# Kernel optimization log

Measured on AMD Instinct MI355X. Metric: run time of the kernel, lower is better.

The kernel has to match this reference:

```python
import jax, jax.numpy as jnp
import numpy as np
from jax import lax

D = 512      # inter_dim
E = 768      # expand_dim
S = 256      # squeeze_dim
BUCKET = 64
N_BLOCK = 6

def layernorm(x, g, b, eps):
    m = jnp.mean(x, axis=-1, keepdims=True)
    v = jnp.mean(jnp.square(x - m), axis=-1, keepdims=True)
    return (x - m) / jnp.sqrt(v + eps) * g + b

def setup_inputs():
    key = jax.random.key(0)
    ks = jax.random.split(key, 12)
    B, N, IN = 4, 4096, 768
    def rn(k, shape, scale):
        return jax.random.normal(k, shape, dtype=jnp.float32) * scale
    return {
        "xs": jax.random.normal(ks[0], (B, N, IN), dtype=jnp.float32),
        # in1: Linear(IN, D) + LayerNorm(eps=1e-8) + LeakyReLU(0.1)
        "W_in": rn(ks[1], (IN, D), IN ** -0.5), "b_in": jnp.zeros(D),
        "ln_in_g": jnp.ones(D), "ln_in_b": jnp.zeros(D),
        # 6 GAU (FlashQuadAttention) blocks, params stacked on leading axis
        "blk_ln_g": jnp.ones((N_BLOCK, D)), "blk_ln_b": jnp.zeros((N_BLOCK, D)),
        "blk_Wuv": rn(ks[2], (N_BLOCK, D, 2 * E + S), D ** -0.5),
        "blk_buv": jnp.zeros((N_BLOCK, 2 * E + S)),
        "blk_gamma": jnp.ones((N_BLOCK, 2, S)) + rn(ks[3], (N_BLOCK, 2, S), 0.02),
        "blk_beta": rn(ks[4], (N_BLOCK, 2, S), 0.02),
        "blk_Wo": rn(ks[5], (N_BLOCK, E, D), E ** -0.5),
        "blk_bo": jnp.zeros((N_BLOCK, D)),
        # tr_layer (applied inside tree loop)
        "tr_W": rn(ks[6], (D, D), D ** -0.5), "tr_b": jnp.zeros(D),
        "tr_a": jnp.full((), 1e-6, dtype=jnp.float32),
        # out1 = TransLayer + Linear(D, out_dim)
        "tr2_W": rn(ks[7], (D, D), D ** -0.5), "tr2_b": jnp.zeros(D),
        "tr2_a": jnp.full((), 1e-6, dtype=jnp.float32),
        "out_W": rn(ks[8], (D, 2), D ** -0.5), "out_b": jnp.zeros(2),
    }

def reference(xs, W_in, b_in, ln_in_g, ln_in_b,
              blk_ln_g, blk_ln_b, blk_Wuv, blk_buv, blk_gamma, blk_beta,
              blk_Wo, blk_bo, tr_W, tr_b, tr_a, tr2_W, tr2_b, tr2_a,
              out_W, out_b):
    def subnet(h):  # h: [n_buckets, BUCKET, D]
        def step(h, p):
            lg, lb, Wuv, buv, gam, bet, Wo, bo = p
            n = layernorm(h, lg, lb, 1e-5)
            uvb = jax.nn.silu(n @ Wuv + buv)
            u, v, base = uvb[..., :E], uvb[..., E:2 * E], uvb[..., 2 * E:]
            q = base * gam[0] + bet[0]
            k = base * gam[1] + bet[1]
            Lq = h.shape[1]
            a = jnp.square(jax.nn.relu(jnp.einsum('gls,gms->glm', q, k) / Lq))
            o = jnp.einsum('glm,gme->gle', a, v) * u
            return h + o @ Wo + bo, None
        h, _ = lax.scan(step, h, (blk_ln_g, blk_ln_b, blk_Wuv, blk_buv,
                                  blk_gamma, blk_beta, blk_Wo, blk_bo))
        return h

    def tr_layer(x, W, b, a):
        return x + jax.nn.gelu(x @ W + b, approximate=False) * a

    def run_sample(x):  # x: [N, in_dim]
        h = layernorm(x @ W_in + b_in, ln_in_g, ln_in_b, 1e-8)
        h = jnp.where(h > 0, h, 0.1 * h)  # LeakyReLU(0.1)
        seq = h
        ys = []
        while seq.shape[0] > 1:  # static shapes -> unrolled tree levels
            ids = jnp.argsort(jnp.linalg.norm(seq, axis=-1))  # sort by L2 norm
            buckets = seq[ids].reshape(-1, BUCKET, D)
            gy = subnet(buckets).mean(axis=1)           # [n_buckets, D]
            ys.append(tr_layer(gy, tr_W, tr_b, tr_a).mean(axis=0))
            seq = gy
        return jnp.stack(ys, 0).mean(0)  # [D]

    y = jax.vmap(run_sample)(xs)          # [B, D]
    y = tr_layer(y, tr2_W, tr2_b, tr2_a)  # out1 TransLayer
    return y @ out_W + out_b              # [B, out_dim]
```

## Files before the change

kernel.cpp:

```cpp
#include <hip/hip_runtime.h>
#include <math.h>

#define R1C 16384

enum { OP_STORE = 0, OP_SILU = 1, OP_RESID = 2, OP_TR = 3 };

typedef _Float16 f16x8 __attribute__((ext_vector_type(8)));
typedef float f32x4 __attribute__((ext_vector_type(4)));

__device__ __forceinline__ float silu_f(float x) { return x / (1.0f + __expf(-x)); }
__device__ __forceinline__ float gelu_f(float x) {
  return 0.5f * x * (1.0f + erff(x * 0.70710678118654752f));
}

__device__ __forceinline__ void gll16(const void* g, const void* l) {
  __builtin_amdgcn_global_load_lds(
      (const __attribute__((address_space(1))) unsigned int*)g,
      (__attribute__((address_space(3))) unsigned int*)l, 16, 0, 0);
}

__device__ __forceinline__ void xcd_swizzle(int& bx, int& by) {
  int nx = gridDim.x;
  int nwg = nx * gridDim.y;
  int flat = by * nx + bx;
  int q = nwg >> 3, r = nwg & 7;
  int xcd = flat & 7, pos = flat >> 3;
  int lbid = (xcd < r) ? xcd * (q + 1) + pos
                       : r * (q + 1) + (xcd - r) * q + pos;
  bx = lbid % nx;
  by = lbid / nx;
}


__global__ __launch_bounds__(512) void gemm_f16(
    const _Float16* __restrict__ A, int lda,
    const _Float16* __restrict__ Bt, int ldb,
    float* __restrict__ C, int ldc, int K,
    const float* __restrict__ bias, int mode,
    const int* __restrict__ ids)
{
  const int BUF = 128 * 32;
  __shared__ _Float16 As[3 * BUF];
  __shared__ _Float16 Bs[3 * BUF];
  int bx = blockIdx.x, by = blockIdx.y;
  xcd_swizzle(bx, by);
  int tid = threadIdx.x;
  int lane = tid & 63, w = tid >> 6;
  int wm = w >> 1, wn = w & 1;
  int row0 = by * 128, col0 = bx * 128;

  int m0 = tid >> 2;
  int k0e = (((tid & 3) - (m0 >> 1)) & 3) * 8;
  const _Float16* gA0 = A + (size_t)(row0 + m0) * lda + k0e;
  const _Float16* gB0 = Bt + (size_t)(col0 + m0) * ldb + k0e;
  const _Float16* lA0 = As + (size_t)(w * 64) * 8;
  const _Float16* lB0 = Bs + (size_t)(w * 64) * 8;

  int mrow = lane & 15, quad = lane >> 4;
  const f16x8* aptr[2];
  const f16x8* bptr[4];
#pragma unroll
  for (int t = 0; t < 2; ++t) {
    int ml = wm * 32 + t * 16 + mrow;
    aptr[t] = (const f16x8*)(As + (size_t)(ml * 4 + ((quad + (ml >> 1)) & 3)) * 8);
  }
#pragma unroll
  for (int nt = 0; nt < 4; ++nt) {
    int nl = wn * 64 + nt * 16 + mrow;
    bptr[nt] = (const f16x8*)(Bs + (size_t)(nl * 4 + ((quad + (nl >> 1)) & 3)) * 8);
  }

  f32x4 acc[2][4] = {};

  int ntile = K >> 5;
  gll16(gA0, lA0); gll16(gB0, lB0);
  gA0 += 32; gB0 += 32;
  if (ntile > 1) {
    gll16(gA0, lA0 + BUF); gll16(gB0, lB0 + BUF);
    gA0 += 32; gB0 += 32;
  }

  int cur = 0;
  for (int t = 0; t < ntile; ++t) {
    if (t + 1 < ntile) asm volatile("s_waitcnt vmcnt(2)" ::: "memory");
    else               asm volatile("s_waitcnt vmcnt(0)" ::: "memory");
    __builtin_amdgcn_s_barrier();
    __builtin_amdgcn_sched_barrier(0);
    if (t + 2 < ntile) {
      int pf = cur + 2; if (pf >= 3) pf -= 3;
      gll16(gA0, lA0 + pf * BUF); gll16(gB0, lB0 + pf * BUF);
      gA0 += 32; gB0 += 32;
    }
    int fo = cur * (BUF / 8);
    f16x8 af[2], bfr[4];
#pragma unroll
    for (int tt = 0; tt < 2; ++tt) af[tt] = *(aptr[tt] + fo);
#pragma unroll
    for (int nt = 0; nt < 4; ++nt) bfr[nt] = *(bptr[nt] + fo);
#pragma unroll
    for (int mt = 0; mt < 2; ++mt)
#pragma unroll
      for (int nt = 0; nt < 4; ++nt)
        acc[mt][nt] = __builtin_amdgcn_mfma_f32_16x16x32_f16(
            af[mt], bfr[nt], acc[mt][nt], 0, 0, 0);
    cur = (cur == 2) ? 0 : cur + 1;
  }

#pragma unroll
  for (int mt = 0; mt < 2; ++mt) {
#pragma unroll
    for (int nt = 0; nt < 4; ++nt) {
      int c = col0 + wn * 64 + nt * 16 + mrow;
      float bv = bias ? bias[c] : 0.0f;
#pragma unroll
      for (int reg = 0; reg < 4; ++reg) {
        int r = row0 + wm * 32 + mt * 16 + quad * 4 + reg;
        float val = acc[mt][nt][reg] + bv;
        if (mode == OP_STORE) {
          C[(size_t)r * ldc + c] = val;
        } else if (mode == OP_SILU) {
          C[(size_t)r * ldc + c] = silu_f(val);
        } else {
          int hr = ids ? ids[r] : r;
          C[(size_t)hr * ldc + c] += val;
        }
      }
    }
  }
}

__global__ __launch_bounds__(512) void gemm_f16_split(
    const _Float16* __restrict__ Ah, const _Float16* __restrict__ Al, int lda,
    const _Float16* __restrict__ Bh, const _Float16* __restrict__ Bl, int ldb,
    float* __restrict__ C, int ldc, int K, const float* __restrict__ bias)
{
  const int BUF = 128 * 32;
  __shared__ _Float16 AsH[2 * BUF], AsL[2 * BUF];
  __shared__ _Float16 BsH[2 * BUF], BsL[2 * BUF];
  int bx = blockIdx.x, by = blockIdx.y;
  xcd_swizzle(bx, by);
  int tid = threadIdx.x;
  int lane = tid & 63, w = tid >> 6;
  int wm = w >> 1, wn = w & 1;
  int row0 = by * 128, col0 = bx * 128;

  int m0 = tid >> 2;
  int k0e = (((tid & 3) - (m0 >> 1)) & 3) * 8;
  size_t a0 = (size_t)(row0 + m0) * lda + k0e;
  size_t b0 = (size_t)(col0 + m0) * ldb + k0e;
  size_t l0 = (size_t)(w * 64) * 8;

  int mrow = lane & 15, quad = lane >> 4;
  size_t aoff[2], boff[4];
#pragma unroll
  for (int t = 0; t < 2; ++t) {
    int ml = wm * 32 + t * 16 + mrow;
    aoff[t] = (size_t)(ml * 4 + ((quad + (ml >> 1)) & 3)) * 8;
  }
#pragma unroll
  for (int nt = 0; nt < 4; ++nt) {
    int nl = wn * 64 + nt * 16 + mrow;
    boff[nt] = (size_t)(nl * 4 + ((quad + (nl >> 1)) & 3)) * 8;
  }

  f32x4 acc[2][4] = {};

  gll16(Ah + a0, AsH + l0); gll16(Al + a0, AsL + l0);
  gll16(Bh + b0, BsH + l0); gll16(Bl + b0, BsL + l0);
  a0 += 32; b0 += 32;

  for (int kt = 0; kt < K; kt += 32) {
    int cur = (kt >> 5) & 1;
    __syncthreads();
    if (kt + 32 < K) {
      size_t o = (size_t)(cur ^ 1) * BUF;
      gll16(Ah + a0, AsH + l0 + o); gll16(Al + a0, AsL + l0 + o);
      gll16(Bh + b0, BsH + l0 + o); gll16(Bl + b0, BsL + l0 + o);
      a0 += 32; b0 += 32;
    }
    size_t o = (size_t)cur * BUF;
    f16x8 ah[2], al_[2], bh[4], bl[4];
#pragma unroll
    for (int t = 0; t < 2; ++t) {
      ah[t]  = *(const f16x8*)(AsH + aoff[t] + o);
      al_[t] = *(const f16x8*)(AsL + aoff[t] + o);
    }
#pragma unroll
    for (int nt = 0; nt < 4; ++nt) {
      bh[nt] = *(const f16x8*)(BsH + boff[nt] + o);
      bl[nt] = *(const f16x8*)(BsL + boff[nt] + o);
    }
#pragma unroll
    for (int mt = 0; mt < 2; ++mt)
#pragma unroll
      for (int nt = 0; nt < 4; ++nt) {
        acc[mt][nt] = __builtin_amdgcn_mfma_f32_16x16x32_f16(
            ah[mt], bh[nt], acc[mt][nt], 0, 0, 0);
        acc[mt][nt] = __builtin_amdgcn_mfma_f32_16x16x32_f16(
            ah[mt], bl[nt], acc[mt][nt], 0, 0, 0);
        acc[mt][nt] = __builtin_amdgcn_mfma_f32_16x16x32_f16(
            al_[mt], bh[nt], acc[mt][nt], 0, 0, 0);
      }
  }

#pragma unroll
  for (int mt = 0; mt < 2; ++mt)
#pragma unroll
    for (int nt = 0; nt < 4; ++nt) {
      int c = col0 + wn * 64 + nt * 16 + mrow;
      float bv = bias ? bias[c] : 0.0f;
#pragma unroll
      for (int reg = 0; reg < 4; ++reg) {
        int r = row0 + wm * 32 + mt * 16 + quad * 4 + reg;
        C[(size_t)r * ldc + c] = acc[mt][nt][reg] + bv;
      }
    }
}

__global__ __launch_bounds__(512) void gemm_f16_uvb(
    const _Float16* __restrict__ A, int lda,
    const _Float16* __restrict__ Bt,
    int c0, int nu,
    _Float16* __restrict__ ub, _Float16* __restrict__ vb, float* __restrict__ baseb,
    int CH, int K, const float* __restrict__ buv)
{
  const int BUF = 128 * 32;
  __shared__ _Float16 As[3 * BUF];
  __shared__ _Float16 Bs[3 * BUF];
  int bx = blockIdx.x, by = blockIdx.y;
  xcd_swizzle(bx, by);
  int tid = threadIdx.x;
  int lane = tid & 63, w = tid >> 6;
  int wm = w >> 1, wn = w & 1;
  int row0 = by * 128;

  int x = bx;
  int xl, regbase, ldc_, is_base = 0;
  _Float16* dst16 = nullptr;
  if (x < nu)            { xl = x;          regbase = c0;        dst16 = ub; ldc_ = CH; }
  else if (x < 2 * nu)   { xl = x - nu;     regbase = 768 + c0;  dst16 = vb; ldc_ = CH; }
  else                   { xl = x - 2 * nu; regbase = 1536;      is_base = 1; ldc_ = 256; }
  int brow0 = regbase + xl * 128;
  int dcol0 = xl * 128;

  int m0 = tid >> 2;
  int k0e = (((tid & 3) - (m0 >> 1)) & 3) * 8;
  const _Float16* gA0 = A + (size_t)(row0 + m0) * lda + k0e;
  const _Float16* gB0 = Bt + (size_t)(brow0 + m0) * 512 + k0e;
  const _Float16* lA0 = As + (size_t)(w * 64) * 8;
  const _Float16* lB0 = Bs + (size_t)(w * 64) * 8;

  int mrow = lane & 15, quad = lane >> 4;
  const f16x8* aptr[2];
  const f16x8* bptr[4];
#pragma unroll
  for (int t = 0; t < 2; ++t) {
    int ml = wm * 32 + t * 16 + mrow;
    aptr[t] = (const f16x8*)(As + (size_t)(ml * 4 + ((quad + (ml >> 1)) & 3)) * 8);
  }
#pragma unroll
  for (int nt = 0; nt < 4; ++nt) {
    int nl = wn * 64 + nt * 16 + mrow;
    bptr[nt] = (const f16x8*)(Bs + (size_t)(nl * 4 + ((quad + (nl >> 1)) & 3)) * 8);
  }

  f32x4 acc[2][4] = {};

  int ntile = K >> 5;
  gll16(gA0, lA0); gll16(gB0, lB0);
  gA0 += 32; gB0 += 32;
  if (ntile > 1) {
    gll16(gA0, lA0 + BUF); gll16(gB0, lB0 + BUF);
    gA0 += 32; gB0 += 32;
  }

  int cur = 0;
  for (int t = 0; t < ntile; ++t) {
    if (t + 1 < ntile) asm volatile("s_waitcnt vmcnt(2)" ::: "memory");
    else               asm volatile("s_waitcnt vmcnt(0)" ::: "memory");
    __builtin_amdgcn_s_barrier();
    __builtin_amdgcn_sched_barrier(0);
    if (t + 2 < ntile) {
      int pf = cur + 2; if (pf >= 3) pf -= 3;
      gll16(gA0, lA0 + pf * BUF); gll16(gB0, lB0 + pf * BUF);
      gA0 += 32; gB0 += 32;
    }
    int fo = cur * (BUF / 8);
    f16x8 af[2], bfr[4];
#pragma unroll
    for (int tt = 0; tt < 2; ++tt) af[tt] = *(aptr[tt] + fo);
#pragma unroll
    for (int nt = 0; nt < 4; ++nt) bfr[nt] = *(bptr[nt] + fo);
#pragma unroll
    for (int mt = 0; mt < 2; ++mt)
#pragma unroll
      for (int nt = 0; nt < 4; ++nt)
        acc[mt][nt] = __builtin_amdgcn_mfma_f32_16x16x32_f16(
            af[mt], bfr[nt], acc[mt][nt], 0, 0, 0);
    cur = (cur == 2) ? 0 : cur + 1;
  }

#pragma unroll
  for (int mt = 0; mt < 2; ++mt) {
#pragma unroll
    for (int nt = 0; nt < 4; ++nt) {
      int lc = wn * 64 + nt * 16 + mrow;
      float bv = buv[brow0 + lc];
#pragma unroll
      for (int reg = 0; reg < 4; ++reg) {
        int r = row0 + wm * 32 + mt * 16 + quad * 4 + reg;
        float val = silu_f(acc[mt][nt][reg] + bv);
        if (is_base) baseb[(size_t)r * 256 + dcol0 + lc] = val;
        else         dst16[(size_t)r * ldc_ + dcol0 + lc] = (_Float16)val;
      }
    }
  }
}

__global__ __launch_bounds__(256) void attnapply_fused(
    const float* __restrict__ base, const float* __restrict__ gb,
    const float* __restrict__ bb, const _Float16* __restrict__ v,
    const _Float16* __restrict__ u, _Float16* __restrict__ t, int CH, int ech)
{
  __shared__ _Float16 smem[3 * 64 * 72];
  _Float16* qs = smem;
  _Float16* ks = smem + 64 * 72;
  _Float16* al = smem + 2 * 64 * 72;
  _Float16* vT = smem;

  int bx = blockIdx.x, by = blockIdx.y;
  xcd_swizzle(bx, by);
  int g = by, tid = threadIdx.x;
  int e_lo = bx * ech, e_hi = e_lo + ech;
  int lane = tid & 63, w = tid >> 6;
  int mrow = lane & 15, quad = lane >> 4;
  int srow = tid >> 2, scol = (tid & 3) * 16;

  f32x4 acc[4] = {};
  for (int s0 = 0; s0 < 256; s0 += 64) {
    const float* bp = base + ((size_t)g * 64 + srow) * 256 + s0 + scol;
#pragma unroll
    for (int j4 = 0; j4 < 4; ++j4) {
      float4 xv = *(const float4*)(bp + j4 * 4);
      float xx[4] = {xv.x, xv.y, xv.z, xv.w};
#pragma unroll
      for (int j = 0; j < 4; ++j) {
        int s = s0 + scol + j4 * 4 + j;
        qs[srow * 72 + scol + j4 * 4 + j] = (_Float16)(xx[j] * gb[s] + bb[s]);
        ks[srow * 72 + scol + j4 * 4 + j] = (_Float16)(xx[j] * gb[256 + s] + bb[256 + s]);
      }
    }
    __syncthreads();
#pragma unroll
    for (int ks2 = 0; ks2 < 2; ++ks2) {
      f16x8 aq = *(const f16x8*)(qs + (w * 16 + mrow) * 72 + ks2 * 32 + quad * 8);
#pragma unroll
      for (int nt = 0; nt < 4; ++nt) {
        f16x8 bk = *(const f16x8*)(ks + (nt * 16 + mrow) * 72 + ks2 * 32 + quad * 8);
        acc[nt] = __builtin_amdgcn_mfma_f32_16x16x32_f16(aq, bk, acc[nt], 0, 0, 0);
      }
    }
    __syncthreads();
  }
#pragma unroll
  for (int nt = 0; nt < 4; ++nt)
#pragma unroll
    for (int reg = 0; reg < 4; ++reg) {
      float val = acc[nt][reg] * (1.0f / 64.0f);
      val = val > 0.0f ? val : 0.0f;
      val = val * val;
      al[(w * 16 + quad * 4 + reg) * 72 + nt * 16 + mrow] = (_Float16)val;
    }
  __syncthreads();

  for (int e0 = e_lo; e0 < e_hi; e0 += 64) {
    const _Float16* vp = v + ((size_t)g * 64 + srow) * CH + e0 + scol;
    f16x8 x0 = *(const f16x8*)vp;
    f16x8 x1 = *(const f16x8*)(vp + 8);
#pragma unroll
    for (int j = 0; j < 8; ++j) {
      vT[(scol + j) * 72 + srow] = x0[j];
      vT[(scol + 8 + j) * 72 + srow] = x1[j];
    }
    __syncthreads();
    f32x4 acc2[4] = {};
#pragma unroll
    for (int ks2 = 0; ks2 < 2; ++ks2) {
      f16x8 af = *(const f16x8*)(al + (w * 16 + mrow) * 72 + ks2 * 32 + quad * 8);
#pragma unroll
      for (int nt = 0; nt < 4; ++nt) {
        f16x8 bf = *(const f16x8*)(vT + (nt * 16 + mrow) * 72 + ks2 * 32 + quad * 8);
        acc2[nt] = __builtin_amdgcn_mfma_f32_16x16x32_f16(af, bf, acc2[nt], 0, 0, 0);
      }
    }
#pragma unroll
    for (int nt = 0; nt < 4; ++nt)
#pragma unroll
      for (int reg = 0; reg < 4; ++reg) {
        int row = w * 16 + quad * 4 + reg;
        int col = e0 + nt * 16 + mrow;
        size_t idx = ((size_t)g * 64 + row) * CH + col;
        t[idx] = (_Float16)(acc2[nt][reg] * (float)u[idx]);
      }
    __syncthreads();
  }
}

__global__ __launch_bounds__(256) void gemm_f32(
    const float* __restrict__ A, int lda,
    const float* __restrict__ B, int ldb,
    float* __restrict__ C, int ldc,
    int M, int N, int K,
    const float* __restrict__ bias, int mode,
    const int* __restrict__ ids,
    const float* __restrict__ X,
    const float* __restrict__ alpha)
{
  __shared__ float As[16][68];
  __shared__ float Bs[16][68];
  int tid = threadIdx.x;
  int tx = tid & 15, ty = tid >> 4;
  int col0 = blockIdx.x * 64, row0 = blockIdx.y * 64;
  float acc[4][4] = {};
  int arow = tid >> 2;
  int ak   = (tid & 3) * 4;
  int bk   = tid >> 4;
  int bn   = (tid & 15) * 4;

  for (int kt = 0; kt < K; kt += 16) {
    float4 av = make_float4(0.f, 0.f, 0.f, 0.f);
    if (row0 + arow < M)
      av = *(const float4*)&A[(size_t)(row0 + arow) * lda + kt + ak];
    As[ak + 0][arow] = av.x; As[ak + 1][arow] = av.y;
    As[ak + 2][arow] = av.z; As[ak + 3][arow] = av.w;
    float4 bv = *(const float4*)&B[(size_t)(kt + bk) * ldb + col0 + bn];
    *(float4*)&Bs[bk][bn] = bv;
    __syncthreads();
#pragma unroll
    for (int k = 0; k < 16; ++k) {
      const float4 a4 = *(const float4*)&As[k][ty * 4];
      const float4 b4 = *(const float4*)&Bs[k][tx * 4];
      float a_[4] = {a4.x, a4.y, a4.z, a4.w};
      float b_[4] = {b4.x, b4.y, b4.z, b4.w};
#pragma unroll
      for (int i = 0; i < 4; ++i)
#pragma unroll
        for (int j = 0; j < 4; ++j)
          acc[i][j] = fmaf(a_[i], b_[j], acc[i][j]);
    }
    __syncthreads();
  }

#pragma unroll
  for (int i = 0; i < 4; ++i) {
    int r = row0 + ty * 4 + i;
    if (r >= M) continue;
#pragma unroll
    for (int j = 0; j < 4; ++j) {
      int c = col0 + tx * 4 + j;
      float val = acc[i][j] + (bias ? bias[c] : 0.0f);
      if (mode == OP_STORE) {
        C[(size_t)r * ldc + c] = val;
      } else if (mode == OP_SILU) {
        C[(size_t)r * ldc + c] = silu_f(val);
      } else if (mode == OP_RESID) {
        int hr = ids ? ids[r] : r;
        C[(size_t)hr * ldc + c] += val;
      } else {
        C[(size_t)r * ldc + c] = X[(size_t)r * ldc + c] + gelu_f(val) * alpha[0];
      }
    }
  }
}

__global__ __launch_bounds__(256) void transpose_cast(
    const float* __restrict__ in, _Float16* __restrict__ out, int K, int N)
{
  in  += (size_t)blockIdx.z * K * N;
  out += (size_t)blockIdx.z * K * N;
  __shared__ float t[32][33];
  int k0 = blockIdx.y * 32, n0 = blockIdx.x * 32;
  int tx = threadIdx.x & 31, ty = threadIdx.x >> 5;
  for (int i = ty; i < 32; i += 8) {
    int k = k0 + i, n = n0 + tx;
    t[i][tx] = (k < K && n < N) ? in[(size_t)k * N + n] : 0.0f;
  }
  __syncthreads();
  for (int i = ty; i < 32; i += 8) {
    int n = n0 + i, k = k0 + tx;
    if (n < N && k < K) out[(size_t)n * K + k] = (_Float16)t[tx][i];
  }
}

__global__ __launch_bounds__(256) void transpose_split(
    const float* __restrict__ in, _Float16* __restrict__ hi,
    _Float16* __restrict__ lo, int K, int N)
{
  __shared__ float t[32][33];
  int k0 = blockIdx.y * 32, n0 = blockIdx.x * 32;
  int tx = threadIdx.x & 31, ty = threadIdx.x >> 5;
  for (int i = ty; i < 32; i += 8) {
    int k = k0 + i, n = n0 + tx;
    t[i][tx] = (k < K && n < N) ? in[(size_t)k * N + n] : 0.0f;
  }
  __syncthreads();
  for (int i = ty; i < 32; i += 8) {
    int n = n0 + i, k = k0 + tx;
    if (n < N && k < K) {
      float x = t[tx][i];
      _Float16 h = (_Float16)x;
      hi[(size_t)n * K + k] = h;
      lo[(size_t)n * K + k] = (_Float16)(x - (float)h);
    }
  }
}

__global__ __launch_bounds__(256) void split_f16_kernel(
    const float* __restrict__ in, _Float16* __restrict__ hi,
    _Float16* __restrict__ lo, int n)
{
  int i = blockIdx.x * 256 + threadIdx.x;
  if (i < n) {
    float x = in[i];
    _Float16 h = (_Float16)x;
    hi[i] = h;
    lo[i] = (_Float16)(x - (float)h);
  }
}

template <typename OUT>
__global__ __launch_bounds__(256) void ln_kernel(
    const float* __restrict__ src, const int* __restrict__ ids,
    OUT* __restrict__ dst, const float* __restrict__ g,
    const float* __restrict__ b, float eps, int leaky,
    float* __restrict__ nrm2)
{
  int r = blockIdx.x;
  int sr = ids ? ids[r] : r;
  int tid = threadIdx.x;
  float v0 = src[(size_t)sr * 512 + tid];
  float v1 = src[(size_t)sr * 512 + tid + 256];
  __shared__ float red[256], red2[256];
  red[tid] = v0 + v1;
  red2[tid] = v0 * v0 + v1 * v1;
  __syncthreads();
  for (int s = 128; s > 0; s >>= 1) {
    if (tid < s) { red[tid] += red[tid + s]; red2[tid] += red2[tid + s]; }
    __syncthreads();
  }
  float mean = red[0] * (1.0f / 512.0f);
  float var  = red2[0] * (1.0f / 512.0f) - mean * mean;
  float rs = rsqrtf(var + eps);
  float o0 = (v0 - mean) * rs * g[tid] + b[tid];
  float o1 = (v1 - mean) * rs * g[tid + 256] + b[tid + 256];
  if (leaky) {
    o0 = o0 > 0.0f ? o0 : 0.1f * o0;
    o1 = o1 > 0.0f ? o1 : 0.1f * o1;
  }
  dst[(size_t)r * 512 + tid] = (OUT)o0;
  dst[(size_t)r * 512 + tid + 256] = (OUT)o1;
  if (nrm2) {
    __syncthreads();
    red[tid] = o0 * o0 + o1 * o1;
    __syncthreads();
    for (int s = 128; s > 0; s >>= 1) {
      if (tid < s) red[tid] += red[tid + s];
      __syncthreads();
    }
    if (tid == 0) nrm2[r] = red[0];
  }
}

__global__ __launch_bounds__(128) void permute_rows(
    const float* __restrict__ src, const int* __restrict__ ids,
    float* __restrict__ dst)
{
  int r = blockIdx.x, sr = ids[r];
  const float4* s = (const float4*)(src + (size_t)sr * 512);
  float4* d = (float4*)(dst + (size_t)r * 512);
  d[threadIdx.x] = s[threadIdx.x];
}

__global__ __launch_bounds__(1024) void sort_kernel(const float* __restrict__ norm2,
                                                    int* __restrict__ ids)
{
  __shared__ float key[4096];
  __shared__ int   val[4096];
  int s = blockIdx.x, tid = threadIdx.x;
  for (int i = tid; i < 4096; i += 1024) { key[i] = norm2[s * 4096 + i]; val[i] = i; }
  __syncthreads();
  for (int len = 2; len <= 4096; len <<= 1) {
    for (int j = len >> 1; j > 0; j >>= 1) {
      for (int t = tid; t < 2048; t += 1024) {
        int i1 = (t << 1) - (t & (j - 1));
        int i2 = i1 + j;
        bool up = ((i1 & len) == 0);
        float ka = key[i1], kb = key[i2];
        int va = val[i1], vb = val[i2];
        bool gt = (ka > kb) || (ka == kb && va > vb);
        if (gt == up) {
          key[i1] = kb; key[i2] = ka;
          val[i1] = vb; val[i2] = va;
        }
      }
      __syncthreads();
    }
  }
  for (int i = tid; i < 4096; i += 1024) ids[s * 4096 + i] = s * 4096 + val[i];
}

__global__ __launch_bounds__(256) void bucketmean_kernel(
    const float* __restrict__ src, const int* __restrict__ ids,
    float* __restrict__ dst)
{
  int g = blockIdx.x, tid = threadIdx.x;
  float s0 = 0.0f, s1 = 0.0f;
  for (int i = 0; i < 64; ++i) {
    int r = g * 64 + i;
    if (ids) r = ids[r];
    s0 += src[(size_t)r * 512 + tid];
    s1 += src[(size_t)r * 512 + tid + 256];
  }
  dst[(size_t)g * 512 + tid] = s0 * (1.0f / 64.0f);
  dst[(size_t)g * 512 + tid + 256] = s1 * (1.0f / 64.0f);
}

__global__ void avg_kernel(const float* __restrict__ a, const float* __restrict__ b,
                           float* __restrict__ o, int n)
{
  int i = blockIdx.x * 256 + threadIdx.x;
  if (i < n) o[i] = 0.5f * (a[i] + b[i]);
}

__global__ void out_kernel(const float* __restrict__ y, const float* __restrict__ W,
                           const float* __restrict__ b, float* __restrict__ out)
{
  int tid = threadIdx.x;
  if (tid < 8) {
    int s = tid >> 1, j = tid & 1;
    float acc = b[j];
    for (int d = 0; d < 512; ++d) acc += y[s * 512 + d] * W[d * 2 + j];
    out[s * 2 + j] = acc;
  }
}

extern "C" void kernel_launch(void* const* d_in, const int* in_sizes, int n_in,
                              void* d_out, int out_size, void* d_ws, size_t ws_size,
                              hipStream_t stream)
{
  const float* xs       = (const float*)d_in[0];
  const float* W_in     = (const float*)d_in[1];
  const float* b_in     = (const float*)d_in[2];
  const float* ln_in_g  = (const float*)d_in[3];
  const float* ln_in_b  = (const float*)d_in[4];
  const float* blk_ln_g = (const float*)d_in[5];
  const float* blk_ln_b = (const float*)d_in[6];
  const float* blk_Wuv  = (const float*)d_in[7];
  const float* blk_buv  = (const float*)d_in[8];
  const float* blk_gam  = (const float*)d_in[9];
  const float* blk_bet  = (const float*)d_in[10];
  const float* blk_Wo   = (const float*)d_in[11];
  const float* blk_bo   = (const float*)d_in[12];
  const float* tr_W     = (const float*)d_in[13];
  const float* tr_b     = (const float*)d_in[14];
  const float* tr_a     = (const float*)d_in[15];
  const float* tr2_W    = (const float*)d_in[16];
  const float* tr2_b    = (const float*)d_in[17];
  const float* tr2_a    = (const float*)d_in[18];
  const float* out_W    = (const float*)d_in[19];
  const float* out_b    = (const float*)d_in[20];
  float* outp = (float*)d_out;

  const size_t R1 = R1C;

  char* wsb = (char*)d_ws;
  size_t off = 0;
  auto carve = [&](size_t bytes) {
    char* r = wsb + off;
    off = (off + bytes + 255) & ~(size_t)255;
    return (void*)r;
  };
  float* h      = (float*)carve(R1 * 512 * 4);
  float* hslot  = (float*)carve(R1 * 512 * 4);
  float* norm2b = (float*)carve(R1 * 4);
  int*   idsb   = (int*)carve(R1 * 4);
  float* gy     = (float*)carve((size_t)256 * 512 * 4);
  float* tl     = (float*)carve((size_t)256 * 512 * 4);
  float* gy2    = (float*)carve(4 * 512 * 4);
  float* ys0    = (float*)carve(4 * 512 * 4);
  float* ys1    = (float*)carve(4 * 512 * 4);
  float* yv     = (float*)carve(4 * 512 * 4);
  float* y2     = (float*)carve(4 * 512 * 4);
  _Float16* Wuvt = (_Float16*)carve((size_t)6 * 1792 * 512 * 2);
  _Float16* Wot  = (_Float16*)carve((size_t)6 * 512 * 768 * 2);
  size_t persistent = off;

  size_t stageA_sorted = 2 * R1 * 768 * 2 + 2 * (size_t)512 * 768 * 2 + R1 * 512 * 4 + 2048;
  size_t block768 = R1 * 256 * 4 + 3 * R1 * (size_t)768 * 2 + 2048;
  size_t un_sorted = stageA_sorted > block768 ? stageA_sorted : block768;
  bool sorted_mode = (persistent + un_sorted + 4096 <= ws_size);

  int CH = 768;
  bool splitA = true;
  if (!sorted_mode) {
    size_t stageA_fb = 2 * R1 * 768 * 2 + 2 * (size_t)512 * 768 * 2 + 1024;
    auto block_bytes = [&](size_t ch) {
      return R1 * 256 * 4 + 3 * R1 * ch * 2 + 2048;
    };
    CH = 0; splitA = false;
    const int cand[4] = {768, 384, 256, 128};
    for (int ci = 0; ci < 4; ++ci) {
      size_t bb2 = block_bytes(cand[ci]);
      size_t un2 = bb2 > stageA_fb ? bb2 : stageA_fb;
      if (persistent + un2 + 4096 <= ws_size) { CH = cand[ci]; splitA = true; break; }
    }
    if (!CH) {
      for (int ci = 0; ci < 4; ++ci)
        if (persistent + block_bytes(cand[ci]) + 4096 <= ws_size) { CH = cand[ci]; break; }
      if (!CH) CH = 128;
    }
  }
  int nu = CH / 128;
  int ech = CH >= 256 ? 256 : CH;
  int nch = CH / ech;

  char* un = wsb + ((persistent + 255) & ~(size_t)255);
  _Float16* xs_hi = (_Float16*)un;
  _Float16* xs_lo = xs_hi + R1 * 768;
  _Float16* Wt_hi = xs_lo + R1 * 768;
  _Float16* Wt_lo = Wt_hi + (size_t)512 * 768;
  float*    nbA   = sorted_mode ? (float*)(Wt_lo + (size_t)512 * 768) : hslot;
  float*    baseb = (float*)un;
  _Float16* ub    = (_Float16*)(un + R1 * 256 * 4);
  _Float16* vb    = ub + R1 * (size_t)CH;
  _Float16* tb    = vb + R1 * (size_t)CH;
  _Float16* nbuf  = sorted_mode ? tb : (_Float16*)hslot;
  float* hres = sorted_mode ? hslot : h;
  const int* blkids = sorted_mode ? nullptr : idsb;

  dim3 blk(256);
  dim3 blk5(512);

  transpose_cast<<<dim3(56, 16, 6), blk, 0, stream>>>(blk_Wuv, Wuvt, 512, 1792);
  transpose_cast<<<dim3(16, 24, 6), blk, 0, stream>>>(blk_Wo, Wot, 768, 512);

  if (splitA) {
    split_f16_kernel<<<(int)(R1 * 768 / 256), blk, 0, stream>>>(xs, xs_hi, xs_lo,
                                                                (int)(R1 * 768));
    transpose_split<<<dim3(16, 24, 1), blk, 0, stream>>>(W_in, Wt_hi, Wt_lo, 768, 512);
    gemm_f16_split<<<dim3(4, 128), blk5, 0, stream>>>(xs_hi, xs_lo, 768,
        Wt_hi, Wt_lo, 768, nbA, 512, 768, b_in);
  } else {
    gemm_f32<<<dim3(8, 256), blk, 0, stream>>>(xs, 768, W_in, 512, nbA, 512,
        16384, 512, 768, b_in, OP_STORE, nullptr, nullptr, nullptr);
  }
  ln_kernel<float><<<16384, 256, 0, stream>>>(nbA, nullptr, h, ln_in_g, ln_in_b,
                                              1e-8f, 1, norm2b);
  sort_kernel<<<4, 1024, 0, stream>>>(norm2b, idsb);
  if (sorted_mode)
    permute_rows<<<16384, 128, 0, stream>>>(h, idsb, hres);

  for (int b = 0; b < 6; ++b) {
    const _Float16* Wuv_t = Wuvt + (size_t)b * 1792 * 512;
    const float*    buv   = blk_buv + b * 1792;
    const _Float16* Wo_t  = Wot + (size_t)b * 512 * 768;
    ln_kernel<_Float16><<<16384, 256, 0, stream>>>(hres, blkids, nbuf,
        blk_ln_g + b * 512, blk_ln_b + b * 512, 1e-5f, 0, nullptr);
    for (int c0 = 0; c0 < 768; c0 += CH) {
      int incl = (c0 == 0) ? 2 : 0;
      gemm_f16_uvb<<<dim3(2 * nu + incl, 128), blk5, 0, stream>>>(nbuf, 512, Wuv_t,
          c0, nu, ub, vb, baseb, CH, 512, buv);
      attnapply_fused<<<dim3(nch, 256), blk, 0, stream>>>(baseb, blk_gam + b * 512,
          blk_bet + b * 512, vb, ub, tb, CH, ech);
      const float* bo = (c0 + CH == 768) ? (blk_bo + b * 512) : nullptr;
      gemm_f16<<<dim3(4, 128), blk5, 0, stream>>>(tb, CH, Wo_t + c0, 768,
          hres, 512, CH, bo, OP_RESID, blkids);
    }
  }
  bucketmean_kernel<<<256, 256, 0, stream>>>(hres, blkids, gy);

  gemm_f32<<<dim3(8, 4), blk, 0, stream>>>(gy, 512, tr_W, 512, tl, 512,
      256, 512, 512, tr_b, OP_TR, nullptr, gy, tr_a);
  bucketmean_kernel<<<4, 256, 0, stream>>>(tl, nullptr, ys0);

  for (int b = 0; b < 6; ++b) {
    const _Float16* Wuv_t = Wuvt + (size_t)b * 1792 * 512;
    const float*    buv   = blk_buv + b * 1792;
    const _Float16* Wo_t  = Wot + (size_t)b * 512 * 768;
    ln_kernel<_Float16><<<256, 256, 0, stream>>>(gy, nullptr, nbuf, blk_ln_g + b * 512,
                                                 blk_ln_b + b * 512, 1e-5f, 0, nullptr);
    for (int c0 = 0; c0 < 768; c0 += CH) {
      int incl = (c0 == 0) ? 2 : 0;
      gemm_f16_uvb<<<dim3(2 * nu + incl, 2), blk5, 0, stream>>>(nbuf, 512, Wuv_t,
          c0, nu, ub, vb, baseb, CH, 512, buv);
      attnapply_fused<<<dim3(nch, 4), blk, 0, stream>>>(baseb, blk_gam + b * 512,
          blk_bet + b * 512, vb, ub, tb, CH, ech);
      const float* bo = (c0 + CH == 768) ? (blk_bo + b * 512) : nullptr;
      gemm_f16<<<dim3(4, 2), blk5, 0, stream>>>(tb, CH, Wo_t + c0, 768,
          gy, 512, CH, bo, OP_RESID, nullptr);
    }
  }
  bucketmean_kernel<<<4, 256, 0, stream>>>(gy, nullptr, gy2);

  gemm_f32<<<dim3(8, 1), blk, 0, stream>>>(gy2, 512, tr_W, 512, ys1, 512,
      4, 512, 512, tr_b, OP_TR, nullptr, gy2, tr_a);
  avg_kernel<<<8, 256, 0, stream>>>(ys0, ys1, yv, 2048);
  gemm_f32<<<dim3(8, 1), blk, 0, stream>>>(yv, 512, tr2_W, 512, y2, 512,
      4, 512, 512, tr2_b, OP_TR, nullptr, yv, tr2_a);
  out_kernel<<<1, 64, 0, stream>>>(y2, out_W, out_b, outp);
}
```

Baseline: 1.595 ms.

## Double-buffer LDS fragment reads in GEMM k-loop to overlap with MFMA

Replaces the per-tile k-loop in the two f16 GEMM kernels with a macro that keeps two register fragment sets. The next tile's LDS fragments are read while MFMAs run on the current one, and global-to-LDS prefetch is issued into the slot just consumed. The aim is to hide LDS read latency behind MFMA issue. The cost is more registers, and the slot reuse and waitcnt logic get harder to keep correct.

After: 1.625 ms. No clear change (+1.9%).

```diff
diff --git a/kernel.cpp b/kernel.cpp
--- a/kernel.cpp
+++ b/kernel.cpp
@@ -32,6 +32,72 @@
 }
 
 
+#define RD_FRAG(Pa0,Pa1,Pb0,Pb1,Pb2,Pb3, slot) do {            \
+    int fo_ = (slot) * (BUF / 8);                               \
+    Pa0 = *(aptr[0] + fo_); Pa1 = *(aptr[1] + fo_);             \
+    Pb0 = *(bptr[0] + fo_); Pb1 = *(bptr[1] + fo_);             \
+    Pb2 = *(bptr[2] + fo_); Pb3 = *(bptr[3] + fo_); } while (0)
+
+#define MM_FRAG(Pa0,Pa1,Pb0,Pb1,Pb2,Pb3) do {                                   \
+    acc[0][0] = __builtin_amdgcn_mfma_f32_16x16x32_f16(Pa0, Pb0, acc[0][0],0,0,0); \
+    acc[0][1] = __builtin_amdgcn_mfma_f32_16x16x32_f16(Pa0, Pb1, acc[0][1],0,0,0); \
+    acc[0][2] = __builtin_amdgcn_mfma_f32_16x16x32_f16(Pa0, Pb2, acc[0][2],0,0,0); \
+    acc[0][3] = __builtin_amdgcn_mfma_f32_16x16x32_f16(Pa0, Pb3, acc[0][3],0,0,0); \
+    acc[1][0] = __builtin_amdgcn_mfma_f32_16x16x32_f16(Pa1, Pb0, acc[1][0],0,0,0); \
+    acc[1][1] = __builtin_amdgcn_mfma_f32_16x16x32_f16(Pa1, Pb1, acc[1][1],0,0,0); \
+    acc[1][2] = __builtin_amdgcn_mfma_f32_16x16x32_f16(Pa1, Pb2, acc[1][2],0,0,0); \
+    acc[1][3] = __builtin_amdgcn_mfma_f32_16x16x32_f16(Pa1, Pb3, acc[1][3],0,0,0); } while (0)
+
+#define STAGE_SLOT(slot) do {                                   \
+    gll16(gA0, lA0 + (slot) * BUF); gll16(gB0, lB0 + (slot) * BUF); \
+    gA0 += 32; gB0 += 32; } while (0)
+
+#define KLOOP_PIPE()                                                     \
+  int ntile = K >> 5;                                                    \
+  STAGE_SLOT(0);                                                         \
+  if (ntile > 1) STAGE_SLOT(1);                                          \
+  if (ntile > 2) STAGE_SLOT(2);                                          \
+  if (ntile > 2) asm volatile("s_waitcnt vmcnt(2)" ::: "memory");        \
+  else           asm volatile("s_waitcnt vmcnt(0)" ::: "memory");        \
+  __builtin_amdgcn_s_barrier();                                          \
+  __builtin_amdgcn_sched_barrier(0);                                     \
+  f16x8 Aa0,Aa1,Ab0,Ab1,Ab2,Ab3, Ba0,Ba1,Bb0,Bb1,Bb2,Bb3;               \
+  RD_FRAG(Aa0,Aa1,Ab0,Ab1,Ab2,Ab3, 0);                                   \
+    \
+                                      \
+  asm volatile("s_waitcnt lgkmcnt(0)" ::: "memory");                     \
+  __builtin_amdgcn_s_barrier();                                          \
+  __builtin_amdgcn_sched_barrier(0);                                     \
+  int scur = 0;                                                          \
+  for (int t = 0; t + 1 < ntile; t += 2) {                               \
+    int s1 = scur + 1; if (s1 == 3) s1 = 0;                              \
+    int s2 = s1 + 1;   if (s2 == 3) s2 = 0;                              \
+                                                         \
+    if (t + 3 < ntile) STAGE_SLOT(scur);                                 \
+    RD_FRAG(Ba0,Ba1,Bb0,Bb1,Bb2,Bb3, s1);                                \
+    MM_FRAG(Aa0,Aa1,Ab0,Ab1,Ab2,Ab3);                                    \
+    if (t + 2 < ntile) {                                                 \
+      asm volatile("s_waitcnt lgkmcnt(0)" ::: "memory");                 \
+      if (t + 3 < ntile) asm volatile("s_waitcnt vmcnt(2)" ::: "memory");\
+      else               asm volatile("s_waitcnt vmcnt(0)" ::: "memory");\
+      __builtin_amdgcn_s_barrier();                                      \
+      __builtin_amdgcn_sched_barrier(0);                                 \
+    }                                                                    \
+                                                       \
+    if (t + 4 < ntile) STAGE_SLOT(s1);                                   \
+    if (t + 2 < ntile) RD_FRAG(Aa0,Aa1,Ab0,Ab1,Ab2,Ab3, s2);             \
+    MM_FRAG(Ba0,Ba1,Bb0,Bb1,Bb2,Bb3);                                    \
+    if (t + 3 < ntile) {                                                 \
+      asm volatile("s_waitcnt lgkmcnt(0)" ::: "memory");                 \
+      if (t + 4 < ntile) asm volatile("s_waitcnt vmcnt(2)" ::: "memory");\
+      else               asm volatile("s_waitcnt vmcnt(0)" ::: "memory");\
+      __builtin_amdgcn_s_barrier();                                      \
+      __builtin_amdgcn_sched_barrier(0);                                 \
+    }                                                                    \
+    scur = s2;                                                           \
+  }                                                                      \
+  if (ntile & 1) MM_FRAG(Aa0,Aa1,Ab0,Ab1,Ab2,Ab3);
+
 __global__ __launch_bounds__(512) void gemm_f16(
     const _Float16* __restrict__ A, int lda,
     const _Float16* __restrict__ Bt, int ldb,
@@ -72,39 +138,7 @@
 
   f32x4 acc[2][4] = {};
 
-  int ntile = K >> 5;
-  gll16(gA0, lA0); gll16(gB0, lB0);
-  gA0 += 32; gB0 += 32;
-  if (ntile > 1) {
-    gll16(gA0, lA0 + BUF); gll16(gB0, lB0 + BUF);
-    gA0 += 32; gB0 += 32;
-  }
-
-  int cur = 0;
-  for (int t = 0; t < ntile; ++t) {
-    if (t + 1 < ntile) asm volatile("s_waitcnt vmcnt(2)" ::: "memory");
-    else               asm volatile("s_waitcnt vmcnt(0)" ::: "memory");
-    __builtin_amdgcn_s_barrier();
-    __builtin_amdgcn_sched_barrier(0);
-    if (t + 2 < ntile) {
-      int pf = cur + 2; if (pf >= 3) pf -= 3;
-      gll16(gA0, lA0 + pf * BUF); gll16(gB0, lB0 + pf * BUF);
-      gA0 += 32; gB0 += 32;
-    }
-    int fo = cur * (BUF / 8);
-    f16x8 af[2], bfr[4];
-#pragma unroll
-    for (int tt = 0; tt < 2; ++tt) af[tt] = *(aptr[tt] + fo);
-#pragma unroll
-    for (int nt = 0; nt < 4; ++nt) bfr[nt] = *(bptr[nt] + fo);
-#pragma unroll
-    for (int mt = 0; mt < 2; ++mt)
-#pragma unroll
-      for (int nt = 0; nt < 4; ++nt)
-        acc[mt][nt] = __builtin_amdgcn_mfma_f32_16x16x32_f16(
-            af[mt], bfr[nt], acc[mt][nt], 0, 0, 0);
-    cur = (cur == 2) ? 0 : cur + 1;
-  }
+  KLOOP_PIPE();
 
 #pragma unroll
   for (int mt = 0; mt < 2; ++mt) {
@@ -266,39 +300,7 @@
 
   f32x4 acc[2][4] = {};
 
-  int ntile = K >> 5;
-  gll16(gA0, lA0); gll16(gB0, lB0);
-  gA0 += 32; gB0 += 32;
-  if (ntile > 1) {
-    gll16(gA0, lA0 + BUF); gll16(gB0, lB0 + BUF);
-    gA0 += 32; gB0 += 32;
-  }
-
-  int cur = 0;
-  for (int t = 0; t < ntile; ++t) {
-    if (t + 1 < ntile) asm volatile("s_waitcnt vmcnt(2)" ::: "memory");
-    else               asm volatile("s_waitcnt vmcnt(0)" ::: "memory");
-    __builtin_amdgcn_s_barrier();
-    __builtin_amdgcn_sched_barrier(0);
-    if (t + 2 < ntile) {
-      int pf = cur + 2; if (pf >= 3) pf -= 3;
-      gll16(gA0, lA0 + pf * BUF); gll16(gB0, lB0 + pf * BUF);
-      gA0 += 32; gB0 += 32;
-    }
-    int fo = cur * (BUF / 8);
-    f16x8 af[2], bfr[4];
-#pragma unroll
-    for (int tt = 0; tt < 2; ++tt) af[tt] = *(aptr[tt] + fo);
-#pragma unroll
-    for (int nt = 0; nt < 4; ++nt) bfr[nt] = *(bptr[nt] + fo);
-#pragma unroll
-    for (int mt = 0; mt < 2; ++mt)
-#pragma unroll
-      for (int nt = 0; nt < 4; ++nt)
-        acc[mt][nt] = __builtin_amdgcn_mfma_f32_16x16x32_f16(
-            af[mt], bfr[nt], acc[mt][nt], 0, 0, 0);
-    cur = (cur == 2) ? 0 : cur + 1;
-  }
+  KLOOP_PIPE();
 
 #pragma unroll
   for (int mt = 0; mt < 2; ++mt) {
```
